# Kernel optimization log

Hardware: AMD Instinct MI355X
Metric: run time of the kernel (lower is better)

Reference implementation:

```python
import jax, jax.numpy as jnp
import numpy as np

# Shapes (match input_specs)
B, C, D, H, W = 1, 2, 64, 112, 112
N = D * H * W
SENT = np.int64(N) * np.int64(N)  # sentinel key, sorts last

# 26-connectivity offsets (for TP/FP/FN components & region graph),
# 6-connectivity offsets (face neighbors, for TN components) -- as in cc3d calls.
OFF26 = [(dz, dy, dx) for dz in (-1, 0, 1) for dy in (-1, 0, 1) for dx in (-1, 0, 1)
         if (dz, dy, dx) != (0, 0, 0)]
OFF6 = {(1, 0, 0), (-1, 0, 0), (0, 1, 0), (0, -1, 0), (0, 0, 1), (0, 0, -1)}


def _shift(a, off, fill):
    """out[i] = a[i+off] if in-bounds else fill. Static pad+slice (jit friendly)."""
    dz, dy, dx = off
    p = jnp.pad(a, 1, constant_values=fill)
    return p[1 + dz:1 + dz + D, 1 + dy:1 + dy + H, 1 + dx:1 + dx + W]


def _label_components(paired):
    """Connected-component labeling of the 4-category paired image.
    Categories: 0=TN (6-conn), 1=FP, 2=FN, 3=TP (26-conn).
    Parallel min-label propagation with pointer-jumping shortcut.
    Final label of each voxel = minimal linear voxel index in its component,
    so labels are unique across categories (components are spatially disjoint)."""
    init = jnp.arange(N, dtype=jnp.int32).reshape(D, H, W)
    big = jnp.int32(N)
    is6 = (paired == 0)

    def nmin(lab):
        m26 = jnp.full((D, H, W), big)
        m6 = jnp.full((D, H, W), big)
        for off in OFF26:
            nl = _shift(lab, off, big)
            same = _shift(paired, off, jnp.int32(-1)) == paired
            cand = jnp.where(same, nl, big)
            m26 = jnp.minimum(m26, cand)
            if off in OFF6:
                m6 = jnp.minimum(m6, cand)
        return jnp.minimum(lab, jnp.where(is6, m6, m26))

    def body(st):
        lab, _ = st
        new = nmin(lab)
        f = new.ravel()
        f = jnp.minimum(f, f[f])  # pointer jump (shortcut) x2 for fast convergence
        f = jnp.minimum(f, f[f])
        new = f.reshape(lab.shape)
        return new, jnp.any(new != lab)

    lab, _ = jax.lax.while_loop(lambda st: st[1], body, (init, jnp.array(True)))
    return lab


def _critical_voxel_mask(paired, labels):
    """Per-voxel mask of critical regions.
    Region graph with 26-connectivity (cc3d.region_graph). A node is critical if
    pred != gt (category 1 or 2) and it does NOT have exactly one correct-fg (TP)
    neighbor component and exactly one correct-bg (TN) neighbor component."""
    pf = paired.ravel()
    keys = []
    for off in OFF26:  # both directions covered since OFF26 is symmetric
        nl = _shift(labels, off, jnp.int32(N))
        valid = (nl != N) & (nl != labels)
        k = jnp.where(valid,
                      labels.astype(jnp.int64) * np.int64(N) + nl.astype(jnp.int64),
                      SENT)
        keys.append(k.ravel())
    keys = jnp.sort(jnp.concatenate(keys))  # [26N] edge keys
    valid = keys < SENT
    uniq = jnp.concatenate([jnp.array([True]), keys[1:] != keys[:-1]]) & valid
    src = jnp.where(valid, (keys // N).astype(jnp.int32), 0)
    dst = jnp.where(valid, (keys % N).astype(jnp.int32), 0)
    dcat = pf[dst]  # category of neighbor component (label == its min voxel index)
    fg_cnt = jax.ops.segment_sum(jnp.where(uniq & (dcat == 3), 1, 0), src, num_segments=N)
    bg_cnt = jax.ops.segment_sum(jnp.where(uniq & (dcat == 0), 1, 0), src, num_segments=N)
    lf = labels.ravel()
    wrong = (pf == 1) | (pf == 2)  # FP or FN component (error_type='all')
    crit = wrong & ~((fg_cnt[lf] == 1) & (bg_cnt[lf] == 1))
    return crit  # [N] bool


def topograph_loss(predictions, targets):
    probs = jax.nn.softmax(predictions, axis=1)
    pred_lab = jnp.argmax(predictions, axis=1)  # hard binarization (thres_var=0)
    reg_sum = jnp.float32(0.0)
    n_reg = jnp.int32(0)
    for b in range(B):
        for c in range(1, C):  # include_background=False
            bin_pred = (pred_lab[b] == c).astype(jnp.int32)
            bin_gt = (targets[b] == c).astype(jnp.int32)
            paired = jax.lax.stop_gradient(bin_pred + 2 * bin_gt)
            labels = _label_components(paired)
            crit = _critical_voxel_mask(paired, labels)
            lf = labels.ravel()
            p = probs[b, c].ravel()
            g = bin_gt.ravel().astype(p.dtype)
            vloss = jnp.where(crit, (p - g) ** 2, 0.0)
            lsum = jax.ops.segment_sum(vloss, lf, num_segments=N)
            ccnt = jax.ops.segment_sum(crit.astype(jnp.int32), lf, num_segments=N)
            # aggregation='mean': mean per critical region, then mean over regions
            reg_sum = reg_sum + jnp.sum(lsum / jnp.maximum(ccnt, 1).astype(lsum.dtype))
            n_reg = n_reg + jnp.sum((ccnt > 0).astype(jnp.int32))
    return jnp.where(n_reg > 0,
                     reg_sum / jnp.maximum(n_reg, 1).astype(jnp.float32),
                     jnp.float32(0.0))


def setup_inputs() -> dict:
    key = jax.random.key(0)
    k1, k2 = jax.random.split(key)
    predictions = jax.random.normal(k1, (B, C, D, H, W), dtype=jnp.float32)
    targets = jax.random.randint(k2, (B, D, H, W), 0, C, dtype=jnp.int32)
    return {"predictions": predictions, "targets": targets}


def reference(predictions, targets):
    return topograph_loss(predictions, targets)
```

## Files before the change

### kernel.cpp

```cpp
#include <hip/hip_runtime.h>
#include <math.h>

#define D_ 64
#define H_ 112
#define W_ 112
#define N_ (D_*H_*W_)
#define HW_ (H_*W_)

#define TX 16
#define TY 16
#define TZ 8
#define TVOX (TX*TY*TZ)
#define NTILES 392

#define PT_BITS 19
#define PT_SLOTS (1 << PT_BITS)
#define PT_MASK (PT_SLOTS - 1)

#define HTS 256


__device__ __forceinline__ int find_root_compress(int* P, int x) {
    int r = P[x];
    if (r == x) return x;
    int p = P[r];
    while (p != r) { r = p; p = P[r]; }
    atomicMin(&P[x], r);
    return r;
}

__device__ __forceinline__ int root_from(const int* __restrict__ P, int p) {
    int q = P[p];
    while (q != p) { p = q; q = P[p]; }
    return p;
}

__device__ __forceinline__ void unite(int* P, int a, int b) {
    while (true) {
        a = find_root_compress(P, a);
        b = find_root_compress(P, b);
        if (a == b) return;
        int hi = a > b ? a : b;
        int lo = a > b ? b : a;
        int old = atomicMin(&P[hi], lo);
        if (old == hi) return;
        a = lo; b = old;
    }
}

__device__ __forceinline__ int lfind(volatile int* L, int x) {
    int p = L[x];
    while (p != x) { x = p; p = L[x]; }
    return x;
}

__device__ __forceinline__ void lunite(int* L, int a, int b) {
    while (true) {
        a = lfind(L, a);
        b = lfind(L, b);
        if (a == b) return;
        int hi = a > b ? a : b;
        int lo = a > b ? b : a;
        int old = atomicMin(&L[hi], lo);
        if (old == hi) return;
        a = lo; b = old;
    }
}

__device__ __forceinline__ void hflush(int lab, int fm, int fx, int bm, int bx,
                                       float v, int c,
                                       int* hkey, int* hfmn, int* hfmx,
                                       int* hbmn, int* hbmx, float* hsum, int* hcnt,
                                       int* fgmin, int* fgmax, int* bgmin, int* bgmax,
                                       double* csum, int* ccnt) {
    unsigned h = ((unsigned)lab * 2654435761u) & (HTS - 1);
    for (int probe = 0; probe < HTS; ++probe) {
        int k = atomicCAS(&hkey[h], -1, lab);
        if (k == -1 || k == lab) {
            if (fx >= 0) { atomicMin(&hfmn[h], fm); atomicMax(&hfmx[h], fx); }
            if (bx >= 0) { atomicMin(&hbmn[h], bm); atomicMax(&hbmx[h], bx); }
            atomicAdd(&hsum[h], v);
            atomicAdd(&hcnt[h], c);
            return;
        }
        h = (h + 1) & (HTS - 1);
    }
    if (fx >= 0) {
        if (fm < fgmin[lab]) atomicMin(&fgmin[lab], fm);
        if (fx > fgmax[lab]) atomicMax(&fgmax[lab], fx);
    }
    if (bx >= 0) {
        if (bm < bgmin[lab]) atomicMin(&bgmin[lab], bm);
        if (bx > bgmax[lab]) atomicMax(&bgmax[lab], bx);
    }
    atomicAdd(&csum[lab], (double)v);
    atomicAdd(&ccnt[lab], c);
}


__global__ __launch_bounds__(512)
void k_local(const float* __restrict__ pred, const int* __restrict__ tgt,
             unsigned char* paired, int* parent,
             unsigned long long* ptab, double* tsum, int* tcnt) {
    __shared__ int L[TVOX];
    __shared__ unsigned char cat[TVOX];
    int tile = blockIdx.x;

    {
        const int PT2 = PT_SLOTS / 2;
        const int per_blk = (PT2 + NTILES - 1) / NTILES;
        int base = tile * per_blk;
        ulonglong2 e; e.x = ~0ULL; e.y = ~0ULL;
        for (int i = threadIdx.x; i < per_blk; i += 512) {
            int idx = base + i;
            if (idx < PT2) ((ulonglong2*)ptab)[idx] = e;
        }
        if (tile == 0 && threadIdx.x == 0) { *tsum = 0.0; *tcnt = 0; }
    }

    int tx = tile % 7, ty = (tile / 7) % 7, tz = tile / 49;
    int bx = tx * TX, by = ty * TY, bz = tz * TZ;

    {
        int i = threadIdx.x * 4;
        int lx = i & 15, ly = (i >> 4) & 15, lz = i >> 8;
        int gv = ((bz + lz) * H_ + by + ly) * W_ + bx + lx;
        float4 a = *(const float4*)&pred[gv];
        float4 b = *(const float4*)&pred[N_ + gv];
        int4 tg = *(const int4*)&tgt[gv];
        float av[4] = {a.x, a.y, a.z, a.w};
        float bv[4] = {b.x, b.y, b.z, b.w};
        int   tv[4] = {tg.x, tg.y, tg.z, tg.w};
        uchar4 pc4;
        unsigned char pcv[4];
        #pragma unroll
        for (int j = 0; j < 4; ++j) {
            int bp = (bv[j] > av[j]) ? 1 : 0;
            int bg = (tv[j] == 1) ? 1 : 0;
            pcv[j] = (unsigned char)(bp + 2 * bg);
        }
        pc4.x = pcv[0]; pc4.y = pcv[1]; pc4.z = pcv[2]; pc4.w = pcv[3];
        *(uchar4*)&paired[gv] = pc4;
        *(uchar4*)&cat[i] = pc4;
        int4 li; li.x = i; li.y = i + 1; li.z = i + 2; li.w = i + 3;
        *(int4*)&L[i] = li;
    }
    __syncthreads();

    for (int i = threadIdx.x; i < TVOX; i += 512) {
        int lx = i & 15, ly = (i >> 4) & 15, lz = i >> 8;
        int c = cat[i];
        if (c == 0) {
            if (lx + 1 < TX && cat[i + 1]   == 0) lunite(L, i, i + 1);
            if (ly + 1 < TY && cat[i + TX]  == 0) lunite(L, i, i + TX);
            if (lz + 1 < TZ && cat[i + 256] == 0) lunite(L, i, i + 256);
        } else {
            #pragma unroll
            for (int dz = 0; dz <= 1; ++dz)
            #pragma unroll
            for (int dy = -1; dy <= 1; ++dy)
            #pragma unroll
            for (int dx = -1; dx <= 1; ++dx) {
                if (dz * 9 + dy * 3 + dx <= 0) continue;
                int nx = lx + dx, ny = ly + dy, nz = lz + dz;
                if (nx < 0 || nx >= TX || ny < 0 || ny >= TY || nz >= TZ) continue;
                int j = i + dz * 256 + dy * TX + dx;
                if (cat[j] == c) lunite(L, i, j);
            }
        }
    }
    __syncthreads();

    {
        int i0 = threadIdx.x * 4;
        int lx = i0 & 15, ly = (i0 >> 4) & 15, lz = i0 >> 8;
        int gv = ((bz + lz) * H_ + by + ly) * W_ + bx + lx;
        int4 grs;
        #pragma unroll
        for (int j = 0; j < 4; ++j) {
            int r = lfind(L, i0 + j);
            int rx = r & 15, ry = (r >> 4) & 15, rz = r >> 8;
            ((int*)&grs)[j] = ((bz + rz) * H_ + by + ry) * W_ + bx + rx;
        }
        *(int4*)&parent[gv] = grs;
    }
}

__global__ void k_border(const unsigned char* __restrict__ paired, int* parent,
                         unsigned long long* ptab) {
    int v = blockIdx.x * blockDim.x + threadIdx.x;
    if (v >= N_) return;
    int x = v % W_;
    int t = v / W_;
    int y = t % H_;
    int z = t / H_;
    int lx = x & 15, ly = y & 15, lz = z & 7;
    if (lx != 0 && lx != 15 && ly != 0 && ly != 15 && lz != 7) return;

    int edges[13];
    int ne = 0;
    int c = paired[v];
    if (c == 0) {
        if (lx == 15 && x + 1 < W_ && paired[v + 1]   == 0) edges[ne++] = v + 1;
        if (ly == 15 && y + 1 < H_ && paired[v + W_]  == 0) edges[ne++] = v + W_;
        if (lz == 7  && z + 1 < D_ && paired[v + HW_] == 0) edges[ne++] = v + HW_;
    } else {
        #pragma unroll
        for (int dz = 0; dz <= 1; ++dz)
        #pragma unroll
        for (int dy = -1; dy <= 1; ++dy)
        #pragma unroll
        for (int dx = -1; dx <= 1; ++dx) {
            if (dz * 9 + dy * 3 + dx <= 0) continue;
            int xx = x + dx, yy = y + dy, zz = z + dz;
            if (zz >= D_ || yy < 0 || yy >= H_ || xx < 0 || xx >= W_) continue;
            if ((xx >> 4) == (x >> 4) && (yy >> 4) == (y >> 4) && (zz >> 3) == (z >> 3))
                continue;
            int u = v + (dz * H_ + dy) * W_ + dx;
            if (paired[u] == c) edges[ne++] = u;
        }
    }
    if (ne == 0) return;
    int ra = parent[v];
    for (int e = 0; e < ne; ++e) {
        int u = edges[e];
        int rb = parent[u];
        if (ra == rb) continue;
        int lo = ra < rb ? ra : rb;
        int hi = ra < rb ? rb : ra;
        unsigned long long key = ((unsigned long long)lo << 20) | (unsigned long long)hi;
        unsigned h = (unsigned)((key * 0x9E3779B97F4A7C15ull) >> 40) & PT_MASK;
        bool doit = true;
        for (int probe = 0; probe < 64; ++probe) {
            unsigned long long cur = ptab[h];
            if (cur == key) { doit = false; break; }
            if (cur == ~0ULL) {
                unsigned long long prev = atomicCAS(&ptab[h], ~0ULL, key);
                if (prev == ~0ULL) break;
                if (prev == key) { doit = false; break; }
            }
            h = (h + 1) & PT_MASK;
        }
        if (doit) unite(parent, lo, hi);
    }
}

__global__ void k_flatten(int* parent, const unsigned char* __restrict__ paired,
                          int* fgmin, int* fgmax, int* bgmin, int* bgmax,
                          double* csum, int* ccnt) {
    int base = (blockIdx.x * blockDim.x + threadIdx.x) * 4;
    if (base >= N_) return;
    int4 p = *(const int4*)&parent[base];
    int4 r;
    r.x = root_from(parent, p.x);
    r.y = root_from(parent, p.y);
    r.z = root_from(parent, p.z);
    r.w = root_from(parent, p.w);
    *(int4*)&parent[base] = r;
    uchar4 cc = *(const uchar4*)&paired[base];
    int rv[4] = {r.x, r.y, r.z, r.w};
    unsigned char cv[4] = {cc.x, cc.y, cc.z, cc.w};
    #pragma unroll
    for (int j = 0; j < 4; ++j) {
        int v = base + j;
        if (rv[j] == v) {
            int c = cv[j];
            if (c == 1 || c == 2) {
                fgmin[v] = N_; fgmax[v] = -1;
                bgmin[v] = N_; bgmax[v] = -1;
                csum[v] = 0.0; ccnt[v] = 0;
            }
        }
    }
}

__global__ void k_scan_acc(const float* __restrict__ pred,
                           const unsigned char* __restrict__ paired,
                           const int* __restrict__ label,
                           int* fgmin, int* fgmax, int* bgmin, int* bgmax,
                           double* csum, int* ccnt) {
    __shared__ int   hkey[HTS];
    __shared__ int   hfmn[HTS], hfmx[HTS], hbmn[HTS], hbmx[HTS];
    __shared__ float hsum[HTS];
    __shared__ int   hcnt[HTS];
    for (int i = threadIdx.x; i < HTS; i += blockDim.x) {
        hkey[i] = -1; hfmn[i] = N_; hfmx[i] = -1; hbmn[i] = N_; hbmx[i] = -1;
        hsum[i] = 0.0f; hcnt[i] = 0;
    }
    __syncthreads();

    int vb = (blockIdx.x * blockDim.x + threadIdx.x) * 4;
    if (vb < N_) {
        uchar4 cc = *(const uchar4*)&paired[vb];
        unsigned char cv[4] = {cc.x, cc.y, cc.z, cc.w};
        bool wrong[4];
        #pragma unroll
        for (int j = 0; j < 4; ++j) wrong[j] = (cv[j] == 1) || (cv[j] == 2);
        bool anyw = wrong[0] || wrong[1] || wrong[2] || wrong[3];
        if (anyw) {
            int x0 = vb % W_;
            int t = vb / W_;
            int y = t % H_;
            int z = t / H_;
            int fmn[4], fmx[4], bmn[4], bmx[4];
            #pragma unroll
            for (int j = 0; j < 4; ++j) { fmn[j] = N_; fmx[j] = -1; bmn[j] = N_; bmx[j] = -1; }

            #pragma unroll
            for (int dz = -1; dz <= 1; ++dz) {
                int zz = z + dz;
                if (zz < 0 || zz >= D_) continue;
                #pragma unroll
                for (int dy = -1; dy <= 1; ++dy) {
                    if (dz == 0 && dy == 0) continue;
                    int yy = y + dy;
                    if (yy < 0 || yy >= H_) continue;
                    int rb = (zz * H_ + yy) * W_ + x0;
                    uchar4 cn = *(const uchar4*)&paired[rb];
                    unsigned char cr[6];
                    cr[1] = cn.x; cr[2] = cn.y; cr[3] = cn.z; cr[4] = cn.w;
                    cr[0] = (x0 > 0)        ? paired[rb - 1] : (unsigned char)255;
                    cr[5] = (x0 + 4 < W_)   ? paired[rb + 4] : (unsigned char)255;
                    #pragma unroll
                    for (int k = 0; k < 6; ++k) {
                        int cu = cr[k];
                        if (cu != 0 && cu != 3) continue;
                        bool need = false;
                        #pragma unroll
                        for (int j = 0; j < 4; ++j)
                            if (j >= k - 2 && j <= k && wrong[j]) need = true;
                        if (!need) continue;
                        int lu = label[rb + k - 1];
                        #pragma unroll
                        for (int j = 0; j < 4; ++j) {
                            if (j < k - 2 || j > k || !wrong[j]) continue;
                            if (cu == 3) { fmn[j] = min(fmn[j], lu); fmx[j] = max(fmx[j], lu); }
                            else         { bmn[j] = min(bmn[j], lu); bmx[j] = max(bmx[j], lu); }
                        }
                    }
                }
            }
            int4 lab4 = *(const int4*)&label[vb];
            int lv[4] = {lab4.x, lab4.y, lab4.z, lab4.w};
            #pragma unroll
            for (int j = 0; j < 4; ++j) {
                if (!wrong[j]) continue;
                #pragma unroll
                for (int jj = 0; jj < 4; ++jj) {
                    if (jj != j - 1 && jj != j + 1) continue;
                    int cu = cv[jj];
                    if (cu == 3) { fmn[j] = min(fmn[j], lv[jj]); fmx[j] = max(fmx[j], lv[jj]); }
                    else if (cu == 0) { bmn[j] = min(bmn[j], lv[jj]); bmx[j] = max(bmx[j], lv[jj]); }
                }
            }
            if (x0 > 0 && wrong[0]) {
                int cu = paired[vb - 1];
                if (cu == 0 || cu == 3) {
                    int lu = label[vb - 1];
                    if (cu == 3) { fmn[0] = min(fmn[0], lu); fmx[0] = max(fmx[0], lu); }
                    else         { bmn[0] = min(bmn[0], lu); bmx[0] = max(bmx[0], lu); }
                }
            }
            if (x0 + 4 < W_ && wrong[3]) {
                int cu = paired[vb + 4];
                if (cu == 0 || cu == 3) {
                    int lu = label[vb + 4];
                    if (cu == 3) { fmn[3] = min(fmn[3], lu); fmx[3] = max(fmx[3], lu); }
                    else         { bmn[3] = min(bmn[3], lu); bmx[3] = max(bmx[3], lu); }
                }
            }

            float4 pa = *(const float4*)&pred[vb];
            float4 pb = *(const float4*)&pred[N_ + vb];
            float va[4] = {pa.x, pa.y, pa.z, pa.w};
            float vbv[4] = {pb.x, pb.y, pb.z, pb.w};
            float val[4];
            #pragma unroll
            for (int j = 0; j < 4; ++j) {
                float p = 1.0f / (1.0f + expf(va[j] - vbv[j]));
                float g = (float)(cv[j] >> 1);
                float d = p - g;
                val[j] = d * d;
            }

            int cl = -1;
            int cfm = N_, cfx = -1, cbm = N_, cbx = -1;
            float cvv = 0.f; int ccc = 0;
            #pragma unroll
            for (int j = 0; j < 4; ++j) {
                if (!wrong[j]) {
                    if (cl >= 0) {
                        hflush(cl, cfm, cfx, cbm, cbx, cvv, ccc,
                               hkey, hfmn, hfmx, hbmn, hbmx, hsum, hcnt,
                               fgmin, fgmax, bgmin, bgmax, csum, ccnt);
                        cl = -1;
                    }
                    continue;
                }
                if (lv[j] == cl) {
                    cfm = min(cfm, fmn[j]); cfx = max(cfx, fmx[j]);
                    cbm = min(cbm, bmn[j]); cbx = max(cbx, bmx[j]);
                    cvv += val[j]; ccc += 1;
                } else {
                    if (cl >= 0)
                        hflush(cl, cfm, cfx, cbm, cbx, cvv, ccc,
                               hkey, hfmn, hfmx, hbmn, hbmx, hsum, hcnt,
                               fgmin, fgmax, bgmin, bgmax, csum, ccnt);
                    cl = lv[j];
                    cfm = fmn[j]; cfx = fmx[j]; cbm = bmn[j]; cbx = bmx[j];
                    cvv = val[j]; ccc = 1;
                }
            }
            if (cl >= 0)
                hflush(cl, cfm, cfx, cbm, cbx, cvv, ccc,
                       hkey, hfmn, hfmx, hbmn, hbmx, hsum, hcnt,
                       fgmin, fgmax, bgmin, bgmax, csum, ccnt);
        }
    }
    __syncthreads();
    for (int i = threadIdx.x; i < HTS; i += blockDim.x) {
        int k = hkey[i];
        if (k >= 0) {
            int a;
            a = hfmn[i]; if (a < N_ && a < fgmin[k]) atomicMin(&fgmin[k], a);
            a = hfmx[i]; if (a >= 0 && a > fgmax[k]) atomicMax(&fgmax[k], a);
            a = hbmn[i]; if (a < N_ && a < bgmin[k]) atomicMin(&bgmin[k], a);
            a = hbmx[i]; if (a >= 0 && a > bgmax[k]) atomicMax(&bgmax[k], a);
            atomicAdd(&csum[k], (double)hsum[i]);
            atomicAdd(&ccnt[k], hcnt[i]);
        }
    }
}

__global__ void k_reduce(const double* __restrict__ csum, const int* __restrict__ ccnt,
                         const int* __restrict__ fgmin, const int* __restrict__ fgmax,
                         const int* __restrict__ bgmin, const int* __restrict__ bgmax,
                         double* tsum, int* tcnt) {
    int base = (blockIdx.x * blockDim.x + threadIdx.x) * 4;
    double s = 0.0; int n = 0;
    if (base < N_) {
        int4 c4 = *(const int4*)&ccnt[base];
        #pragma unroll
        for (int j = 0; j < 4; ++j) {
            int c = (j == 0) ? c4.x : (j == 1) ? c4.y : (j == 2) ? c4.z : c4.w;
            if (c > 0) {
                int l = base + j;
                int fmn = fgmin[l], fmx = fgmax[l], bmn = bgmin[l], bmx = bgmax[l];
                bool ok = (fmn < N_) && (fmn == fmx) && (bmn < N_) && (bmn == bmx);
                if (!ok) {
                    s += csum[l] / (double)c;
                    n++;
                }
            }
        }
    }
    #pragma unroll
    for (int o = 32; o > 0; o >>= 1) {
        s += __shfl_down(s, o);
        n += __shfl_down(n, o);
    }
    __shared__ double sh_s[4];
    __shared__ int    sh_n[4];
    int wid = threadIdx.x >> 6;
    int lane = threadIdx.x & 63;
    if (lane == 0) { sh_s[wid] = s; sh_n[wid] = n; }
    __syncthreads();
    if (threadIdx.x == 0) {
        double S = sh_s[0] + sh_s[1] + sh_s[2] + sh_s[3];
        int    M = sh_n[0] + sh_n[1] + sh_n[2] + sh_n[3];
        if (M) { atomicAdd(tsum, S); atomicAdd(tcnt, M); }
    }
}

__global__ void k_final(const double* __restrict__ tsum, const int* __restrict__ tcnt,
                        float* out) {
    int n = *tcnt;
    out[0] = (n > 0) ? (float)(*tsum / (double)n) : 0.0f;
}


extern "C" void kernel_launch(void* const* d_in, const int* in_sizes, int n_in,
                              void* d_out, int out_size, void* d_ws, size_t ws_size,
                              hipStream_t stream) {
    const float* pred = (const float*)d_in[0];
    const int*   tgt  = (const int*)d_in[1];
    float* out = (float*)d_out;

    char* ws = (char*)d_ws;
    const size_t N4 = (size_t)4 * N_;
    int*           parent = (int*)(ws + 0 * N4);
    int*           fgmin  = (int*)(ws + 1 * N4);
    int*           fgmax  = (int*)(ws + 2 * N4);
    int*           bgmin  = (int*)(ws + 3 * N4);
    int*           bgmax  = (int*)(ws + 4 * N4);
    int*           ccnt   = (int*)(ws + 5 * N4);
    double*        csum   = (double*)(ws + 6 * N4);
    unsigned char* paired = (unsigned char*)(ws + 8 * N4);
    double*        tsum   = (double*)(ws + 8 * N4 + N_);
    int*           tcnt   = (int*)(ws + 8 * N4 + N_ + 8);
    unsigned long long* ptab = (unsigned long long*)(ws + 8 * N4 + N_ + 16);

    const int TPB = 256;
    const int NB = (N_ + TPB - 1) / TPB;
    const int NB4 = (N_ / 4 + TPB - 1) / TPB;

    k_local<<<NTILES, 512, 0, stream>>>(pred, tgt, paired, parent, ptab, tsum, tcnt);
    k_border<<<NB, TPB, 0, stream>>>(paired, parent, ptab);
    k_flatten<<<NB4, TPB, 0, stream>>>(parent, paired,
                                       fgmin, fgmax, bgmin, bgmax, csum, ccnt);
    k_scan_acc<<<NB4, TPB, 0, stream>>>(pred, paired, parent,
                                        fgmin, fgmax, bgmin, bgmax, csum, ccnt);
    k_reduce<<<NB4, TPB, 0, stream>>>(csum, ccnt,
                                      fgmin, fgmax, bgmin, bgmax, tsum, tcnt);
    k_final<<<1, 1, 0, stream>>>(tsum, tcnt, out);
}
```

Measured before the change: 234.6 us.

## Prune redundant diagonal unions and compress paths in tile-local labeling

The in-tile union-find now gives each thread four contiguous voxels and reuses their categories from registers instead of a strided loop. For 26-connected categories it skips diagonal and corner unions when the two voxels are already linked through shared face or edge neighbours of the same category. The find used during union now compresses paths with an atomicMin. This is meant to cut the number of atomic union operations and the length of root chains in the local labeling pass. The cost is more shared-memory category reads per voxel and more branch divergence.

```diff
diff --git a/kernel.cpp b/kernel.cpp
--- a/kernel.cpp
+++ b/kernel.cpp
@@ -48,6 +48,15 @@
     }
 }
 
+__device__ __forceinline__ int lfindc(int* L, int x) {
+    int r = L[x];
+    if (r == x) return x;
+    int p = L[r];
+    while (p != r) { r = p; p = L[r]; }
+    atomicMin(&L[x], r);
+    return r;
+}
+
 __device__ __forceinline__ int lfind(volatile int* L, int x) {
     int p = L[x];
     while (p != x) { x = p; p = L[x]; }
@@ -56,8 +65,8 @@
 
 __device__ __forceinline__ void lunite(int* L, int a, int b) {
     while (true) {
-        a = lfind(L, a);
-        b = lfind(L, b);
+        a = lfindc(L, a);
+        b = lfindc(L, b);
         if (a == b) return;
         int hi = a > b ? a : b;
         int lo = a > b ? b : a;
@@ -121,60 +130,79 @@
     int tx = tile % 7, ty = (tile / 7) % 7, tz = tile / 49;
     int bx = tx * TX, by = ty * TY, bz = tz * TZ;
 
+    int i0 = threadIdx.x * 4;
+    int lx0 = i0 & 15, ly = (i0 >> 4) & 15, lz = i0 >> 8;
+    int gv0 = ((bz + lz) * H_ + by + ly) * W_ + bx + lx0;
+    unsigned char pcv[4];
+
     {
-        int i = threadIdx.x * 4;
-        int lx = i & 15, ly = (i >> 4) & 15, lz = i >> 8;
-        int gv = ((bz + lz) * H_ + by + ly) * W_ + bx + lx;
-        float4 a = *(const float4*)&pred[gv];
-        float4 b = *(const float4*)&pred[N_ + gv];
-        int4 tg = *(const int4*)&tgt[gv];
+        float4 a = *(const float4*)&pred[gv0];
+        float4 b = *(const float4*)&pred[N_ + gv0];
+        int4 tg = *(const int4*)&tgt[gv0];
         float av[4] = {a.x, a.y, a.z, a.w};
         float bv[4] = {b.x, b.y, b.z, b.w};
         int   tv[4] = {tg.x, tg.y, tg.z, tg.w};
-        uchar4 pc4;
-        unsigned char pcv[4];
         #pragma unroll
         for (int j = 0; j < 4; ++j) {
             int bp = (bv[j] > av[j]) ? 1 : 0;
             int bg = (tv[j] == 1) ? 1 : 0;
             pcv[j] = (unsigned char)(bp + 2 * bg);
         }
-        pc4.x = pcv[0]; pc4.y = pcv[1]; pc4.z = pcv[2]; pc4.w = pcv[3];
-        *(uchar4*)&paired[gv] = pc4;
-        *(uchar4*)&cat[i] = pc4;
-        int4 li; li.x = i; li.y = i + 1; li.z = i + 2; li.w = i + 3;
-        *(int4*)&L[i] = li;
+        uchar4 pc4; pc4.x = pcv[0]; pc4.y = pcv[1]; pc4.z = pcv[2]; pc4.w = pcv[3];
+        *(uchar4*)&paired[gv0] = pc4;
+        *(uchar4*)&cat[i0] = pc4;
+        int4 li; li.x = i0; li.y = i0 + 1; li.z = i0 + 2; li.w = i0 + 3;
+        *(int4*)&L[i0] = li;
     }
     __syncthreads();
 
-    for (int i = threadIdx.x; i < TVOX; i += 512) {
-        int lx = i & 15, ly = (i >> 4) & 15, lz = i >> 8;
-        int c = cat[i];
+    #pragma unroll
+    for (int j = 0; j < 4; ++j) {
+        int i = i0 + j;
+        int lx = lx0 + j;
+        int c = pcv[j];
         if (c == 0) {
-            if (lx + 1 < TX && cat[i + 1]   == 0) lunite(L, i, i + 1);
-            if (ly + 1 < TY && cat[i + TX]  == 0) lunite(L, i, i + TX);
-            if (lz + 1 < TZ && cat[i + 256] == 0) lunite(L, i, i + 256);
+            if (lx < 15 && cat[i + 1]   == 0) lunite(L, i, i + 1);
+            if (ly < 15 && cat[i + 16]  == 0) lunite(L, i, i + 16);
+            if (lz < 7  && cat[i + 256] == 0) lunite(L, i, i + 256);
         } else {
-            #pragma unroll
-            for (int dz = 0; dz <= 1; ++dz)
-            #pragma unroll
-            for (int dy = -1; dy <= 1; ++dy)
-            #pragma unroll
-            for (int dx = -1; dx <= 1; ++dx) {
-                if (dz * 9 + dy * 3 + dx <= 0) continue;
-                int nx = lx + dx, ny = ly + dy, nz = lz + dz;
-                if (nx < 0 || nx >= TX || ny < 0 || ny >= TY || nz >= TZ) continue;
-                int j = i + dz * 256 + dy * TX + dx;
-                if (cat[j] == c) lunite(L, i, j);
-            }
+            bool xp = lx < 15, xm = lx > 0, yp = ly < 15, ym = ly > 0, zp = lz < 7;
+            if (xp && cat[i + 1]   == c) lunite(L, i, i + 1);
+            if (yp && cat[i + 16]  == c) lunite(L, i, i + 16);
+            if (zp && cat[i + 256] == c) lunite(L, i, i + 256);
+            if (xp && yp && cat[i + 17] == c &&
+                !(cat[i + 1] == c || cat[i + 16] == c)) lunite(L, i, i + 17);
+            if (xm && yp && cat[i + 15] == c &&
+                !(cat[i - 1] == c || cat[i + 16] == c)) lunite(L, i, i + 15);
+            if (xp && zp && cat[i + 257] == c &&
+                !(cat[i + 1] == c || cat[i + 256] == c)) lunite(L, i, i + 257);
+            if (xm && zp && cat[i + 255] == c &&
+                !(cat[i - 1] == c || cat[i + 256] == c)) lunite(L, i, i + 255);
+            if (yp && zp && cat[i + 272] == c &&
+                !(cat[i + 16] == c || cat[i + 256] == c)) lunite(L, i, i + 272);
+            if (ym && zp && cat[i + 240] == c &&
+                !(cat[i - 16] == c || cat[i + 256] == c)) lunite(L, i, i + 240);
+            if (xp && yp && zp && cat[i + 273] == c &&
+                !((cat[i + 1] == c && cat[i + 17] == c) ||
+                  (cat[i + 16] == c && cat[i + 17] == c) ||
+                  (cat[i + 256] == c && cat[i + 257] == c))) lunite(L, i, i + 273);
+            if (xm && yp && zp && cat[i + 271] == c &&
+                !((cat[i - 1] == c && cat[i + 15] == c) ||
+                  (cat[i + 16] == c && cat[i + 15] == c) ||
+                  (cat[i + 256] == c && cat[i + 255] == c))) lunite(L, i, i + 271);
+            if (xp && ym && zp && cat[i + 241] == c &&
+                !((cat[i + 1] == c && cat[i - 15] == c) ||
+                  (cat[i - 16] == c && cat[i - 15] == c) ||
+                  (cat[i + 256] == c && cat[i + 257] == c))) lunite(L, i, i + 241);
+            if (xm && ym && zp && cat[i + 239] == c &&
+                !((cat[i - 1] == c && cat[i - 17] == c) ||
+                  (cat[i - 16] == c && cat[i - 17] == c) ||
+                  (cat[i + 256] == c && cat[i + 255] == c))) lunite(L, i, i + 239);
         }
     }
     __syncthreads();
 
     {
-        int i0 = threadIdx.x * 4;
-        int lx = i0 & 15, ly = (i0 >> 4) & 15, lz = i0 >> 8;
-        int gv = ((bz + lz) * H_ + by + ly) * W_ + bx + lx;
         int4 grs;
         #pragma unroll
         for (int j = 0; j < 4; ++j) {
@@ -182,7 +210,7 @@
             int rx = r & 15, ry = (r >> 4) & 15, rz = r >> 8;
             ((int*)&grs)[j] = ((bz + rz) * H_ + by + ry) * W_ + bx + rx;
         }
-        *(int4*)&parent[gv] = grs;
+        *(int4*)&parent[gv0] = grs;
     }
 }
 
```

Result: faster. 218.7 us (-6.8%).
